# Performance work log

Measured on AMD Instinct MI355X. Metric: run time of the kernel, lower is better.

Reference implementation:

```python
import jax, jax.numpy as jnp
import numpy as np

N_NODES = 100000


def gcn_conv(x, edge_index, W, b, n):
    """PyG-style GCNConv: h = D^-1/2 (A + I) D^-1/2 (x W) + b."""
    h = x @ W  # [n, out]
    loops = jnp.arange(n, dtype=edge_index.dtype)
    src = jnp.concatenate([edge_index[0], loops])
    dst = jnp.concatenate([edge_index[1], loops])
    deg = jax.ops.segment_sum(jnp.ones_like(dst, dtype=h.dtype), dst, num_segments=n)
    dinv = jnp.where(deg > 0, jax.lax.rsqrt(deg), 0.0)
    norm = dinv[src] * dinv[dst]  # [E+n]
    msg = h[src] * norm[:, None]
    out = jax.ops.segment_sum(msg, dst, num_segments=n)
    return out + b


def setup_inputs() -> dict:
    key = jax.random.key(0)
    ks = jax.random.split(key, 12)
    n, f, hid, c, e = N_NODES, 128, 16, 32, 3200000
    x = jax.random.normal(ks[0], (n, f), dtype=jnp.float32)
    edge_index_pos = jax.random.randint(ks[1], (2, e), 0, n, dtype=jnp.int32)
    edge_index_neg = jax.random.randint(ks[2], (2, e), 0, n, dtype=jnp.int32)
    def glorot(k, fi, fo):
        lim = np.sqrt(6.0 / (fi + fo)).astype(np.float32)
        return jax.random.uniform(k, (fi, fo), minval=-lim, maxval=lim, dtype=jnp.float32)
    return {
        "x": x,
        "edge_index_pos": edge_index_pos,
        "edge_index_neg": edge_index_neg,
        "W1p": glorot(ks[3], f, hid), "b1p": jnp.zeros((hid,), jnp.float32),
        "W1n": glorot(ks[4], f, hid), "b1n": jnp.zeros((hid,), jnp.float32),
        "W2p": glorot(ks[5], hid, c), "b2p": jnp.zeros((c,), jnp.float32),
        "W2n": glorot(ks[6], hid, c), "b2n": jnp.zeros((c,), jnp.float32),
    }


def reference(x, edge_index_pos, edge_index_neg, W1p, b1p, W1n, b1n, W2p, b2p, W2n, b2n):
    n = x.shape[0]
    # layer 1: relu(pos) - relu(neg)
    h = (jax.nn.relu(gcn_conv(x, edge_index_pos, W1p, b1p, n))
         - jax.nn.relu(gcn_conv(x, edge_index_neg, W1n, b1n, n)))
    # dropout is identity in eval mode (training=False)
    h = (jax.nn.relu(gcn_conv(h, edge_index_pos, W2p, b2p, n))
         - jax.nn.relu(gcn_conv(h, edge_index_neg, W2n, b2n, n)))
    return jax.nn.log_softmax(h, axis=1)
```

## Files before the change

kernel.cpp:

```cpp
#include <hip/hip_runtime.h>
#include <hip/hip_fp16.h>


#define BSHIFT 8
#define BSZ 256
#define MAX_NBK 512
#define FILL_CAP 6272
#define SORT_CAP 10240

typedef int   i32x4 __attribute__((ext_vector_type(4)));

__device__ __forceinline__ int chunk_of_block(int bid, int NCH) {
  return (NCH % 8 == 0) ? (bid % 8) * (NCH / 8) + bid / 8 : bid;
}


__global__ __launch_bounds__(256) void bucket_count2(
    const int* __restrict__ eP, const int* __restrict__ eN,
    int E, int CH, int NCH, int NBK, int* __restrict__ ccP, int* __restrict__ ccN) {
  __shared__ int cnt[MAX_NBK][2];
  const int* dsts = (blockIdx.y ? eN : eP) + E;
  int* cc = blockIdx.y ? ccN : ccP;
  const int c = chunk_of_block(blockIdx.x, NCH);
  for (int i = threadIdx.x; i < NBK * 2; i += 256) ((int*)cnt)[i] = 0;
  __syncthreads();
  const int sub = threadIdx.x & 1;
  int base = c * CH, end = min(E, base + CH);
  for (int idx = base + threadIdx.x * 4; idx < end; idx += 1024) {
    if (idx + 4 <= end) {
      i32x4 d = __builtin_nontemporal_load((const i32x4*)(dsts + idx));
      atomicAdd(&cnt[d.x >> BSHIFT][sub], 1);
      atomicAdd(&cnt[d.y >> BSHIFT][sub], 1);
      atomicAdd(&cnt[d.z >> BSHIFT][sub], 1);
      atomicAdd(&cnt[d.w >> BSHIFT][sub], 1);
    } else {
      for (int k = idx; k < end; ++k) atomicAdd(&cnt[dsts[k] >> BSHIFT][sub], 1);
    }
  }
  __syncthreads();
  for (int i = threadIdx.x; i < NBK; i += 256)
    cc[(size_t)c * NBK + i] = cnt[i][0] + cnt[i][1];
}

__global__ __launch_bounds__(512) void col_scan2(
    int* __restrict__ ccP, int* __restrict__ ccN, int NCH, int NBK,
    int* __restrict__ totP, int* __restrict__ totN) {
  __shared__ int s[512];
  int* cc = blockIdx.y ? ccN : ccP;
  int* tot = blockIdx.y ? totN : totP;
  int b = blockIdx.x, t = threadIdx.x;
  int v = (t < NCH) ? cc[(size_t)t * NBK + b] : 0;
  s[t] = v;
  for (int off = 1; off < 512; off <<= 1) {
    __syncthreads();
    int a = (t >= off) ? s[t - off] : 0;
    __syncthreads();
    s[t] += a;
  }
  __syncthreads();
  if (t < NCH) cc[(size_t)t * NBK + b] = s[t] - v;
  if (t == 511) tot[b] = s[511];
}

__global__ __launch_bounds__(512) void bucket_fill3(
    const int* __restrict__ eP, const int* __restrict__ eN,
    int E, int CH, int NCH, int NBK,
    const int* __restrict__ ccP, const int* __restrict__ ccN,
    const int* __restrict__ totP, const int* __restrict__ totN,
    unsigned* __restrict__ prP, unsigned* __restrict__ prN) {
  __shared__ unsigned obuf[FILL_CAP];
  __shared__ int chofs[MAX_NBK], hist[MAX_NBK], lofs[MAX_NBK], cur[MAX_NBK];
  __shared__ int bas_l[MAX_NBK];
  __shared__ int s[512];
  const int* edges = blockIdx.y ? eN : eP;
  const int* cc = blockIdx.y ? ccN : ccP;
  const int* tot = blockIdx.y ? totN : totP;
  unsigned* pairs = blockIdx.y ? prN : prP;
  const int c = chunk_of_block(blockIdx.x, NCH);
  const int t = threadIdx.x;

  int h = 0;
  if (t < NBK) {
    int o0 = cc[(size_t)c * NBK + t];
    int o1 = (c + 1 < NCH) ? cc[(size_t)(c + 1) * NBK + t] : tot[t];
    chofs[t] = o0;
    h = o1 - o0;
    hist[t] = h;
  }
  s[t] = h;
  for (int off = 1; off < 512; off <<= 1) {
    __syncthreads();
    int a = (t >= off) ? s[t - off] : 0;
    __syncthreads();
    s[t] += a;
  }
  __syncthreads();
  if (t < NBK) { lofs[t] = s[t] - hist[t]; cur[t] = s[t] - hist[t]; }
  __syncthreads();

  int tv = (t < NBK) ? tot[t] : 0;
  s[t] = tv;
  for (int off = 1; off < 512; off <<= 1) {
    __syncthreads();
    int a = (t >= off) ? s[t - off] : 0;
    __syncthreads();
    s[t] += a;
  }
  __syncthreads();
  if (t < NBK) bas_l[t] = s[t] - tv;
  __syncthreads();

  int base = c * CH, end = min(E, base + CH);
  for (int idx = base + t * 4; idx < end; idx += 2048) {
    if (idx + 4 <= end) {
      i32x4 sv = __builtin_nontemporal_load((const i32x4*)(edges + idx));
      i32x4 dv = __builtin_nontemporal_load((const i32x4*)(edges + E + idx));
      int p0 = atomicAdd(&cur[dv.x >> BSHIFT], 1);
      obuf[p0] = (unsigned)sv.x | ((unsigned)(dv.x & (BSZ - 1)) << 24);
      int p1 = atomicAdd(&cur[dv.y >> BSHIFT], 1);
      obuf[p1] = (unsigned)sv.y | ((unsigned)(dv.y & (BSZ - 1)) << 24);
      int p2 = atomicAdd(&cur[dv.z >> BSHIFT], 1);
      obuf[p2] = (unsigned)sv.z | ((unsigned)(dv.z & (BSZ - 1)) << 24);
      int p3 = atomicAdd(&cur[dv.w >> BSHIFT], 1);
      obuf[p3] = (unsigned)sv.w | ((unsigned)(dv.w & (BSZ - 1)) << 24);
    } else {
      for (int k = idx; k < end; ++k) {
        int sv = edges[k], d = edges[E + k];
        int pos = atomicAdd(&cur[d >> BSHIFT], 1);
        obuf[pos] = (unsigned)sv | ((unsigned)(d & (BSZ - 1)) << 24);
      }
    }
  }
  __syncthreads();

  const int wv = t >> 5, ln = t & 31;
  for (int b = wv; b < NBK; b += 16) {
    int cnt2 = hist[b], lo = lofs[b];
    unsigned* dst = pairs + (size_t)bas_l[b] + chofs[b];
    for (int j = ln; j < cnt2; j += 32) dst[j] = obuf[lo + j];
  }
}

__global__ __launch_bounds__(256) void tile_sort3(
    const unsigned* __restrict__ prP, const unsigned* __restrict__ prN,
    const int* __restrict__ totP, const int* __restrict__ totN, int n, int E,
    float* __restrict__ dinvP, float* __restrict__ dinvN,
    int* __restrict__ rowP, int* __restrict__ rowN,
    unsigned* __restrict__ srcsP, unsigned* __restrict__ srcsN) {
  __shared__ unsigned obuf[SORT_CAP];
  __shared__ int hist4[BSZ][4];
  __shared__ int scn[BSZ];
  __shared__ int cur[BSZ];
  __shared__ int red[256];
  const unsigned* pairs = blockIdx.y ? prN : prP;
  const int* tot = blockIdx.y ? totN : totP;
  float* dinv = blockIdx.y ? dinvN : dinvP;
  int* rowoff = blockIdx.y ? rowN : rowP;
  unsigned* srcs = blockIdx.y ? srcsN : srcsP;
  const int b = blockIdx.x, t = threadIdx.x;

  int part = 0;
  for (int j = t; j < b; j += 256) part += tot[j];
  red[t] = part;
  for (int i = t; i < BSZ * 4; i += 256) ((int*)hist4)[i] = 0;
  __syncthreads();
  for (int off = 128; off > 0; off >>= 1) {
    if (t < off) red[t] += red[t + off];
    __syncthreads();
  }
  const int s0 = red[0];
  const int cnt = tot[b];
  const int s1 = s0 + cnt;
  if (b == (int)gridDim.x - 1 && t == 0) rowoff[n] = E;

  const int sub = t & 3;
  for (int i = s0 + t; i < s1; i += 256)
    atomicAdd(&hist4[pairs[i] >> 24][sub], 1);
  __syncthreads();
  const int h = hist4[t][0] + hist4[t][1] + hist4[t][2] + hist4[t][3];
  scn[t] = h;
  __syncthreads();
  for (int off = 1; off < BSZ; off <<= 1) {
    int v = (t >= off) ? scn[t - off] : 0;
    __syncthreads();
    scn[t] += v;
    __syncthreads();
  }
  {
    int excl = scn[t] - h;
    cur[t] = excl;
    int node = b * BSZ + t;
    if (node < n) {
      rowoff[node] = s0 + excl;
      dinv[node] = rsqrtf(1.0f + (float)h);
    }
  }
  __syncthreads();
  if (cnt <= SORT_CAP) {
    for (int i = s0 + t; i < s1; i += 256) {
      unsigned p = __builtin_nontemporal_load(pairs + i);
      int pos = atomicAdd(&cur[p >> 24], 1);
      obuf[pos] = p & 0xFFFFFFu;
    }
    __syncthreads();
    for (int i = t; i < cnt; i += 256) srcs[s0 + i] = obuf[i];
  } else {
    for (int i = s0 + t; i < s1; i += 256) {
      unsigned p = __builtin_nontemporal_load(pairs + i);
      int pos = atomicAdd(&cur[p >> 24], 1);
      srcs[s0 + pos] = p & 0xFFFFFFu;
    }
  }
}

__global__ __launch_bounds__(256) void xw1_kernel(
    const float* __restrict__ x, const float* __restrict__ Wp, const float* __restrict__ Wn,
    const float* __restrict__ dinvP, const float* __restrict__ dinvN,
    __half* __restrict__ hp, __half* __restrict__ hn, int n)
{
  __shared__ float xs[16 * 132];
  __shared__ float wp[128 * 16], wn[128 * 16];
  const int tid = threadIdx.x;
  const int rowBase = blockIdx.x * 16;

  for (int idx = tid; idx < 512; idx += 256) {
    ((float4*)wp)[idx] = ((const float4*)Wp)[idx];
    ((float4*)wn)[idx] = ((const float4*)Wn)[idx];
  }
  const int nrows = min(16, n - rowBase);
  for (int idx = tid; idx < nrows * 32; idx += 256) {
    int r = idx >> 5, c4 = idx & 31;
    float4 v = ((const float4*)(x + (size_t)(rowBase + r) * 128))[c4];
    *(float4*)(xs + r * 132 + c4 * 4) = v;
  }
  __syncthreads();

  const int r = tid >> 4, c = tid & 15;
  const int i = rowBase + r;
  if (i < n) {
    float ap = 0.f, an = 0.f;
    #pragma unroll
    for (int k = 0; k < 128; ++k) {
      float xv = xs[r * 132 + k];
      ap += xv * wp[k * 16 + c];
      an += xv * wn[k * 16 + c];
    }
    hp[(size_t)i * 16 + c] = __float2half(ap * dinvP[i]);
    hn[(size_t)i * 16 + c] = __float2half(an * dinvN[i]);
  }
}

__device__ __forceinline__ void fma_mix2(float& aLo, float& aHi, unsigned h2, float one) {
  asm("v_fma_mix_f32 %0, %2, %3, %0 op_sel:[0,0,0] op_sel_hi:[1,0,0]\n\t"
      "v_fma_mix_f32 %1, %2, %3, %1 op_sel:[1,0,0] op_sel_hi:[1,0,0]"
      : "+v"(aLo), "+v"(aHi)
      : "v"(h2), "v"(one));
}

__device__ __forceinline__ void seg_sum4(
    const unsigned* __restrict__ srcs, int e, int e1,
    const __half* __restrict__ tab, int lane4, float one,
    float& f0, float& f1, float& f2, float& f3)
{
  float g0 = 0.f, g1 = 0.f, g2 = 0.f, g3 = 0.f;
  for (; e + 8 <= e1; e += 8) {
    unsigned a[8];
    #pragma unroll
    for (int j = 0; j < 8; ++j) a[j] = srcs[e + j];
    uint2 v[8];
    #pragma unroll
    for (int j = 0; j < 8; ++j)
      v[j] = *(const uint2*)(tab + (size_t)a[j] * 16 + lane4 * 4);
    #pragma unroll
    for (int j = 0; j < 8; j += 2) {
      fma_mix2(f0, f1, v[j].x, one);
      fma_mix2(f2, f3, v[j].y, one);
      fma_mix2(g0, g1, v[j + 1].x, one);
      fma_mix2(g2, g3, v[j + 1].y, one);
    }
  }
  for (; e + 2 <= e1; e += 2) {
    unsigned a0 = srcs[e], a1 = srcs[e + 1];
    uint2 v0 = *(const uint2*)(tab + (size_t)a0 * 16 + lane4 * 4);
    uint2 v1 = *(const uint2*)(tab + (size_t)a1 * 16 + lane4 * 4);
    fma_mix2(f0, f1, v0.x, one);
    fma_mix2(f2, f3, v0.y, one);
    fma_mix2(g0, g1, v1.x, one);
    fma_mix2(g2, g3, v1.y, one);
  }
  if (e < e1) {
    uint2 v = *(const uint2*)(tab + (size_t)srcs[e] * 16 + lane4 * 4);
    fma_mix2(f0, f1, v.x, one);
    fma_mix2(f2, f3, v.y, one);
  }
  f0 += g0; f1 += g1; f2 += g2; f3 += g3;
}

__global__ __launch_bounds__(256) void agg_split(
    const unsigned* __restrict__ srcP, const int* __restrict__ rowP,
    const unsigned* __restrict__ srcN, const int* __restrict__ rowN,
    const __half* __restrict__ inP, const __half* __restrict__ inN,
    const float* __restrict__ dinvP, const float* __restrict__ dinvN,
    float* __restrict__ tmpP, float* __restrict__ tmpN, int n)
{
  const int gb = blockIdx.x;
  const int xcd = gb & 7;
  const int sign = xcd >> 2;
  const int nblk = (gb >> 3) * 4 + (xcd & 3);
  const int lane4 = threadIdx.x & 3, grp = threadIdx.x >> 2;
  const int i = nblk * 64 + grp;
  if (i >= n) return;

  const unsigned* __restrict__ srcs = sign ? srcN : srcP;
  const int* __restrict__ row = sign ? rowN : rowP;
  const __half* __restrict__ tab = sign ? inN : inP;
  const float* __restrict__ dinv = sign ? dinvN : dinvP;
  float* __restrict__ tmp = sign ? tmpN : tmpP;

  const float one = 1.0f;
  float f0 = 0.f, f1 = 0.f, f2 = 0.f, f3 = 0.f;
  uint2 self = *(const uint2*)(tab + (size_t)i * 16 + lane4 * 4);
  fma_mix2(f0, f1, self.x, one);
  fma_mix2(f2, f3, self.y, one);
  seg_sum4(srcs, row[i], row[i + 1], tab, lane4, one, f0, f1, f2, f3);
  const float d = dinv[i];
  float4 o;
  o.x = f0 * d; o.y = f1 * d; o.z = f2 * d; o.w = f3 * d;
  *(float4*)(tmp + (size_t)i * 16 + lane4 * 4) = o;
}

__global__ __launch_bounds__(256) void combine1(
    const float* __restrict__ tmpP, const float* __restrict__ tmpN,
    const float* __restrict__ bp, const float* __restrict__ bn,
    const float* __restrict__ dinvP, const float* __restrict__ dinvN,
    __half* __restrict__ Gp, __half* __restrict__ Gn, int nq)
{
  int q = blockIdx.x * 256 + threadIdx.x;
  if (q >= nq) return;
  int i = q >> 2;
  float4 tp = ((const float4*)tmpP)[q];
  float4 tn = ((const float4*)tmpN)[q];
  float4 bpv = ((const float4*)bp)[q & 3];
  float4 bnv = ((const float4*)bn)[q & 3];
  float dp = dinvP[i], dn = dinvN[i];
  float h0 = fmaxf(bpv.x + tp.x, 0.f) - fmaxf(bnv.x + tn.x, 0.f);
  float h1 = fmaxf(bpv.y + tp.y, 0.f) - fmaxf(bnv.y + tn.y, 0.f);
  float h2 = fmaxf(bpv.z + tp.z, 0.f) - fmaxf(bnv.z + tn.z, 0.f);
  float h3 = fmaxf(bpv.w + tp.w, 0.f) - fmaxf(bnv.w + tn.w, 0.f);
  union { uint2 u; __half2 h[2]; } a, b;
  a.h[0] = __floats2half2_rn(h0 * dp, h1 * dp);
  a.h[1] = __floats2half2_rn(h2 * dp, h3 * dp);
  b.h[0] = __floats2half2_rn(h0 * dn, h1 * dn);
  b.h[1] = __floats2half2_rn(h2 * dn, h3 * dn);
  ((uint2*)Gp)[q] = a.u;
  ((uint2*)Gn)[q] = b.u;
}

__global__ __launch_bounds__(256) void final2(
    const float* __restrict__ Up, const float* __restrict__ Un,
    const float* __restrict__ W2p, const float* __restrict__ W2n,
    const float* __restrict__ b2p, const float* __restrict__ b2n,
    float* __restrict__ out, int n)
{
  __shared__ float wp[16 * 32], wn[16 * 32];
  for (int i = threadIdx.x; i < 512; i += 256) { wp[i] = W2p[i]; wn[i] = W2n[i]; }
  __syncthreads();

  const int tid = threadIdx.x;
  const int lane = tid & 15, grp = tid >> 4;
  const int i = blockIdx.x * 16 + grp;
  if (i >= n) return;

  float tp = Up[(size_t)i * 16 + lane];
  float tn = Un[(size_t)i * 16 + lane];

  float ap0 = b2p[lane], ap1 = b2p[lane + 16];
  float an0 = b2n[lane], an1 = b2n[lane + 16];
  #pragma unroll
  for (int k = 0; k < 16; ++k) {
    float tpk = __shfl(tp, k, 16);
    float tnk = __shfl(tn, k, 16);
    ap0 += tpk * wp[k * 32 + lane];
    ap1 += tpk * wp[k * 32 + lane + 16];
    an0 += tnk * wn[k * 32 + lane];
    an1 += tnk * wn[k * 32 + lane + 16];
  }
  float v0 = fmaxf(ap0, 0.f) - fmaxf(an0, 0.f);
  float v1 = fmaxf(ap1, 0.f) - fmaxf(an1, 0.f);
  float m = fmaxf(v0, v1);
  #pragma unroll
  for (int off = 8; off > 0; off >>= 1) m = fmaxf(m, __shfl_xor(m, off, 16));
  float s = __expf(v0 - m) + __expf(v1 - m);
  #pragma unroll
  for (int off = 8; off > 0; off >>= 1) s += __shfl_xor(s, off, 16);
  float ls = __logf(s);
  out[(size_t)i * 32 + lane] = v0 - m - ls;
  out[(size_t)i * 32 + lane + 16] = v1 - m - ls;
}

extern "C" void kernel_launch(void* const* d_in, const int* in_sizes, int n_in,
                              void* d_out, int out_size, void* d_ws, size_t ws_size,
                              hipStream_t stream) {
  const float* x   = (const float*)d_in[0];
  const int*   eP  = (const int*)d_in[1];
  const int*   eN  = (const int*)d_in[2];
  const float* W1p = (const float*)d_in[3];
  const float* b1p = (const float*)d_in[4];
  const float* W1n = (const float*)d_in[5];
  const float* b1n = (const float*)d_in[6];
  const float* W2p = (const float*)d_in[7];
  const float* b2p = (const float*)d_in[8];
  const float* W2n = (const float*)d_in[9];
  const float* b2n = (const float*)d_in[10];
  float* out = (float*)d_out;

  const int HID = in_sizes[4];
  const int F   = in_sizes[3] / HID;
  const int n   = in_sizes[0] / F;
  const int E   = in_sizes[1] / 2;
  (void)out_size; (void)n_in; (void)ws_size;

  const int NBK = (n + BSZ - 1) >> BSHIFT;
  const int CH  = (((E + 511) / 512) + 3) & ~3;
  const int NCH = (E + CH - 1) / CH;

  char* p = (char*)d_ws;
  auto alloc = [&](size_t bytes) { char* r = p; p += (bytes + 255) & ~(size_t)255; return r; };

  int*      ccP   = (int*)alloc((size_t)NCH * NBK * 4);
  int*      ccN   = (int*)alloc((size_t)NCH * NBK * 4);
  int*      totP  = (int*)alloc((size_t)NBK * 4);
  int*      totN  = (int*)alloc((size_t)NBK * 4);
  unsigned* prP   = (unsigned*)alloc((size_t)E * 4);
  unsigned* prN   = (unsigned*)alloc((size_t)E * 4);
  unsigned* srcP  = (unsigned*)alloc((size_t)E * 4);
  unsigned* srcN  = (unsigned*)alloc((size_t)E * 4);
  int*      rowP  = (int*)alloc((size_t)(n + 1) * 4);
  int*      rowN  = (int*)alloc((size_t)(n + 1) * 4);
  float*    dinvP = (float*)alloc((size_t)n * 4);
  float*    dinvN = (float*)alloc((size_t)n * 4);
  __half*   hsP   = (__half*)alloc((size_t)n * 16 * 2);
  __half*   hsN   = (__half*)alloc((size_t)n * 16 * 2);
  __half*   Gp    = (__half*)alloc((size_t)n * 16 * 2);
  __half*   Gn    = (__half*)alloc((size_t)n * 16 * 2);
  float*    tmpP  = (float*)alloc((size_t)n * 16 * 4);
  float*    tmpN  = (float*)alloc((size_t)n * 16 * 4);

  hipLaunchKernelGGL(bucket_count2, dim3(NCH, 2), dim3(256), 0, stream,
                     eP, eN, E, CH, NCH, NBK, ccP, ccN);
  hipLaunchKernelGGL(col_scan2, dim3(NBK, 2), dim3(512), 0, stream,
                     ccP, ccN, NCH, NBK, totP, totN);
  hipLaunchKernelGGL(bucket_fill3, dim3(NCH, 2), dim3(512), 0, stream,
                     eP, eN, E, CH, NCH, NBK, ccP, ccN, totP, totN, prP, prN);
  hipLaunchKernelGGL(tile_sort3, dim3(NBK, 2), dim3(256), 0, stream,
                     prP, prN, totP, totN, n, E, dinvP, dinvN, rowP, rowN, srcP, srcN);

  const int NB16 = (n + 15) / 16;
  const int NB64 = (n + 63) / 64;
  const int NBS  = ((NB64 + 3) / 4) * 4;
  const int GRID = NBS * 2;

  hipLaunchKernelGGL(xw1_kernel, dim3(NB16), dim3(256), 0, stream,
                     x, W1p, W1n, dinvP, dinvN, hsP, hsN, n);
  hipLaunchKernelGGL(agg_split, dim3(GRID), dim3(256), 0, stream,
                     srcP, rowP, srcN, rowN, hsP, hsN, dinvP, dinvN, tmpP, tmpN, n);
  hipLaunchKernelGGL(combine1, dim3((n * 4 + 255) / 256), dim3(256), 0, stream,
                     tmpP, tmpN, b1p, b1n, dinvP, dinvN, Gp, Gn, n * 4);

  hipLaunchKernelGGL(agg_split, dim3(GRID), dim3(256), 0, stream,
                     srcP, rowP, srcN, rowN, Gp, Gn, dinvP, dinvN, tmpP, tmpN, n);
  hipLaunchKernelGGL(final2, dim3(NB16), dim3(256), 0, stream,
                     tmpP, tmpN, W2p, W2n, b2p, b2n, out, n);
}
```

Measured before the change: 227.7 us.

## Tile column scan over 32 buckets per block and cache dst loads

The column scan now handles 32 buckets per block. Each block loads a 32-column tile of chunk counts with coalesced row reads, scans it in shared memory, and writes back exclusive prefixes and totals, where before each block strided through memory for a single bucket. Separately, the destination-index loads in the count and fill kernels switch from nontemporal to normal loads, so the second read of dst can hit in cache. The tile uses 64KB of shared memory and 32-element register arrays, which may cut occupancy, and the scan takes log2(NCH) rounds over the whole tile.

```diff
diff --git a/kernel.cpp b/kernel.cpp
--- a/kernel.cpp
+++ b/kernel.cpp
@@ -28,7 +28,7 @@
   int base = c * CH, end = min(E, base + CH);
   for (int idx = base + threadIdx.x * 4; idx < end; idx += 1024) {
     if (idx + 4 <= end) {
-      i32x4 d = __builtin_nontemporal_load((const i32x4*)(dsts + idx));
+      i32x4 d = *(const i32x4*)(dsts + idx);
       atomicAdd(&cnt[d.x >> BSHIFT][sub], 1);
       atomicAdd(&cnt[d.y >> BSHIFT][sub], 1);
       atomicAdd(&cnt[d.z >> BSHIFT][sub], 1);
@@ -45,21 +45,41 @@
 __global__ __launch_bounds__(512) void col_scan2(
     int* __restrict__ ccP, int* __restrict__ ccN, int NCH, int NBK,
     int* __restrict__ totP, int* __restrict__ totN) {
-  __shared__ int s[512];
+  __shared__ int tile[512][32];
   int* cc = blockIdx.y ? ccN : ccP;
   int* tot = blockIdx.y ? totN : totP;
-  int b = blockIdx.x, t = threadIdx.x;
-  int v = (t < NCH) ? cc[(size_t)t * NBK + b] : 0;
-  s[t] = v;
-  for (int off = 1; off < 512; off <<= 1) {
-    __syncthreads();
-    int a = (t >= off) ? s[t - off] : 0;
-    __syncthreads();
-    s[t] += a;
-  }
-  __syncthreads();
-  if (t < NCH) cc[(size_t)t * NBK + b] = s[t] - v;
-  if (t == 511) tot[b] = s[511];
+  const int b0 = blockIdx.x * 32;
+  const int t = threadIdx.x;
+
+  for (int i = t; i < NCH * 32; i += 512) {
+    int r = i >> 5, c = i & 31, b = b0 + c;
+    tile[r][c] = (b < NBK) ? cc[(size_t)r * NBK + b] : 0;
+  }
+  __syncthreads();
+
+  for (int off = 1; off < NCH; off <<= 1) {
+    int a[32];
+    #pragma unroll
+    for (int k = 0; k < 32; ++k) {
+      int i = t + k * 512;
+      int r = i >> 5, c = i & 31;
+      a[k] = (i < NCH * 32 && r >= off) ? tile[r - off][c] : 0;
+    }
+    __syncthreads();
+    #pragma unroll
+    for (int k = 0; k < 32; ++k) {
+      int i = t + k * 512;
+      int r = i >> 5, c = i & 31;
+      if (i < NCH * 32) tile[r][c] += a[k];
+    }
+    __syncthreads();
+  }
+
+  for (int i = t; i < NCH * 32; i += 512) {
+    int r = i >> 5, c = i & 31, b = b0 + c;
+    if (b < NBK) cc[(size_t)r * NBK + b] = r ? tile[r - 1][c] : 0;
+  }
+  if (t < 32 && b0 + t < NBK) tot[b0 + t] = tile[NCH - 1][t];
 }
 
 __global__ __launch_bounds__(512) void bucket_fill3(
@@ -114,7 +134,7 @@
   for (int idx = base + t * 4; idx < end; idx += 2048) {
     if (idx + 4 <= end) {
       i32x4 sv = __builtin_nontemporal_load((const i32x4*)(edges + idx));
-      i32x4 dv = __builtin_nontemporal_load((const i32x4*)(edges + E + idx));
+      i32x4 dv = *(const i32x4*)(edges + E + idx);
       int p0 = atomicAdd(&cur[dv.x >> BSHIFT], 1);
       obuf[p0] = (unsigned)sv.x | ((unsigned)(dv.x & (BSZ - 1)) << 24);
       int p1 = atomicAdd(&cur[dv.y >> BSHIFT], 1);
@@ -448,7 +468,7 @@
 
   hipLaunchKernelGGL(bucket_count2, dim3(NCH, 2), dim3(256), 0, stream,
                      eP, eN, E, CH, NCH, NBK, ccP, ccN);
-  hipLaunchKernelGGL(col_scan2, dim3(NBK, 2), dim3(512), 0, stream,
+  hipLaunchKernelGGL(col_scan2, dim3((NBK + 31) / 32, 2), dim3(512), 0, stream,
                      ccP, ccN, NCH, NBK, totP, totN);
   hipLaunchKernelGGL(bucket_fill3, dim3(NCH, 2), dim3(512), 0, stream,
                      eP, eN, E, CH, NCH, NBK, ccP, ccN, totP, totN, prP, prN);
```

Result: slower. 252.1 us (+10.7%).
